# Kernel tuning notes

Hardware: AMD Instinct MI355X
Metric: run time of the kernel (lower is better)

## Reference

```python
import jax, jax.numpy as jnp
import numpy as np

B, H, NI, NQ = 4096, 1024, 4096, 2048


def setup_inputs() -> dict:
    key = jax.random.key(0)
    ks = jax.random.split(key, 12)
    state = jax.random.normal(ks[0], (B, H), jnp.float32)
    inputX = jax.random.normal(ks[1], (B, NI), jnp.float32)
    # one-hot next-question vector
    q_idx = jax.random.randint(ks[2], (B,), 0, NQ)
    inputY = jax.nn.one_hot(q_idx, NQ, dtype=jnp.float32)
    truth = jax.random.bernoulli(ks[3], 0.5, (B,)).astype(jnp.float32)
    # torch.nn.Linear default init: U(-1/sqrt(fan_in), 1/sqrt(fan_in)), weight (out,in)
    def lin(kw, kb, out_d, in_d):
        bound = 1.0 / np.sqrt(in_d)
        W = jax.random.uniform(kw, (out_d, in_d), jnp.float32, -bound, bound)
        b = jax.random.uniform(kb, (out_d,), jnp.float32, -bound, bound)
        return W, b
    W_t, b_t = lin(ks[4], ks[5], H, H)    # transfer: n_hidden -> n_hidden
    W_x, b_x = lin(ks[6], ks[7], H, NI)   # linear_x: n_input -> n_hidden
    W_y, b_y = lin(ks[8], ks[9], NQ, H)   # linear_y: n_hidden -> n_questions
    return {"state": state, "inputX": inputX, "inputY": inputY, "truth": truth,
            "W_t": W_t, "b_t": b_t, "W_x": W_x, "b_x": b_x, "W_y": W_y, "b_y": b_y}


def reference(state, inputX, inputY, truth, W_t, b_t, W_x, b_x, W_y, b_y):
    # two small linears + tanh -> new hidden state
    linM = state @ W_t.T + b_t                       # (B, H)
    linX = inputX @ W_x.T + b_x                      # (B, H)
    hidden = jnp.tanh(linM + linX)                   # (B, H)
    # prediction head: linear + sigmoid, mask-select via one-hot sum
    pred_output = jax.nn.sigmoid(hidden @ W_y.T + b_y)  # (B, NQ)
    pred = jnp.sum(pred_output * inputY, axis=1)        # (B,)
    # binary cross entropy, sum reduction; torch clamps log terms at -100
    log_p = jnp.maximum(jnp.log(pred), -100.0)
    log_1mp = jnp.maximum(jnp.log1p(-pred), -100.0)
    err = -jnp.sum(truth * log_p + (1.0 - truth) * log_1mp)
    return (pred, err, hidden)
```

## Files before the change

### kernel.cpp

```cpp
#include <hip/hip_runtime.h>
#include <stdint.h>
#include <math.h>

#define B_DIM 4096
#define H_DIM 1024
#define NI_DIM 4096
#define NQ_DIM 2048
#define K_DIM 5120
#define NKT 160

typedef __attribute__((ext_vector_type(8))) short short8;
typedef __attribute__((ext_vector_type(4))) float f32x4;

__device__ __forceinline__ unsigned short f2bf(float f) {
  unsigned u = __float_as_uint(f);
  u += 0x7FFFu + ((u >> 16) & 1u);
  return (unsigned short)(u >> 16);
}

__device__ __forceinline__ void gload_lds16(const void* g, void* l) {
  __builtin_amdgcn_global_load_lds(
      (__attribute__((address_space(1))) void*)(uintptr_t)g,
      (__attribute__((address_space(3))) void*)l, 16, 0, 0);
}

__global__ __launch_bounds__(256) void cast_tile(
    const float* __restrict__ src0, const float* __restrict__ src1,
    short* __restrict__ dst) {
  __shared__ __align__(16) short lds[4096];
  const unsigned bt = blockIdx.x;
  const int rowTile = bt / NKT;
  const int kt = bt % NKT;
  const float* src;
  long long srcBase;
  int cols;
  if (kt < 32) { src = src0; cols = 1024; srcBase = (long long)kt * 32; }
  else         { src = src1; cols = 4096; srcBase = (long long)(kt - 32) * 32; }
  const int tid = threadIdx.x;
#pragma unroll
  for (int half = 0; half < 2; ++half) {
    int c = tid + half * 256;
    int r = c >> 2, s = c & 3;
    long long sa = ((long long)(rowTile * 128 + r)) * cols + srcBase + s * 8;
    float4 v0 = *(const float4*)(src + sa);
    float4 v1 = *(const float4*)(src + sa + 4);
    short8 o;
    o[0] = (short)f2bf(v0.x); o[1] = (short)f2bf(v0.y);
    o[2] = (short)f2bf(v0.z); o[3] = (short)f2bf(v0.w);
    o[4] = (short)f2bf(v1.x); o[5] = (short)f2bf(v1.y);
    o[6] = (short)f2bf(v1.z); o[7] = (short)f2bf(v1.w);
    *(short8*)(&lds[(s * 128 + r) * 8]) = o;
  }
  __syncthreads();
  short* dtile = dst + (((long long)rowTile * NKT + kt) * 512) * 8;
#pragma unroll
  for (int half = 0; half < 2; ++half) {
    int c = tid + half * 256;
    *(short8*)(dtile + c * 8) = *(const short8*)(&lds[c * 8]);
  }
}

__global__ __launch_bounds__(256, 4) void gemm_splitk(
    const short* __restrict__ Xc, const short* __restrict__ Wc,
    float* __restrict__ P, int ntk) {
  __shared__ __align__(16) short As[2][4096];
  __shared__ __align__(16) short Bs[2][4096];
  const int tid = threadIdx.x;
  const int lane = tid & 63;
  const int wid = tid >> 6;
  const int wm = wid >> 1, wn = wid & 1;
  const int fr = lane & 15, fq = lane >> 4;

  const int nwg = gridDim.x;
  const int orig = blockIdx.x;
  const int cpx = nwg >> 3;
  const int swz = (orig & 7) * cpx + (orig >> 3);
  const int bz = swz >> 8;
  const int bm = (swz >> 3) & 31;
  const int bn = swz & 7;
  const int kt0 = bz * ntk;

  const int c0 = tid, c1 = tid + 256;
  const short* gA = Xc + (((long long)bm * NKT + kt0) << 12);
  const short* gB = Wc + (((long long)bn * NKT + kt0) << 12);

  f32x4 acc[4][4] = {};

  gload_lds16(gA + c0 * 8, &As[0][c0 * 8]);
  gload_lds16(gA + c1 * 8, &As[0][c1 * 8]);
  gload_lds16(gB + c0 * 8, &Bs[0][c0 * 8]);
  gload_lds16(gB + c1 * 8, &Bs[0][c1 * 8]);
  __syncthreads();

  int cur = 0;
  for (int t = 0; t < ntk; ++t) {
    if (t + 1 < ntk) {
      const short* nA = gA + (t + 1) * 4096;
      const short* nB = gB + (t + 1) * 4096;
      gload_lds16(nA + c0 * 8, &As[cur ^ 1][c0 * 8]);
      gload_lds16(nA + c1 * 8, &As[cur ^ 1][c1 * 8]);
      gload_lds16(nB + c0 * 8, &Bs[cur ^ 1][c0 * 8]);
      gload_lds16(nB + c1 * 8, &Bs[cur ^ 1][c1 * 8]);
    }
    const short* a_base = &As[cur][0];
    const short* b_base = &Bs[cur][0];
    short8 av[4], bv[4];
#pragma unroll
    for (int i = 0; i < 4; i++) {
      av[i] = *(const short8*)(a_base + (fq * 128 + wm * 64 + i * 16 + fr) * 8);
      bv[i] = *(const short8*)(b_base + (fq * 128 + wn * 64 + i * 16 + fr) * 8);
    }
#pragma unroll
    for (int mi = 0; mi < 4; mi++)
#pragma unroll
      for (int ni = 0; ni < 4; ni++)
        acc[mi][ni] = __builtin_amdgcn_mfma_f32_16x16x32_bf16(
            av[mi], bv[ni], acc[mi][ni], 0, 0, 0);
    __syncthreads();
    cur ^= 1;
  }

  float* Pp = P + (long long)bz * B_DIM * H_DIM;
  const int row0 = bm * 128 + wm * 64;
  const int col0 = bn * 128 + wn * 64;
#pragma unroll
  for (int ni = 0; ni < 4; ni++) {
    int col = col0 + ni * 16 + fr;
#pragma unroll
    for (int mi = 0; mi < 4; mi++) {
#pragma unroll
      for (int r = 0; r < 4; r++) {
        int row = row0 + mi * 16 + fq * 4 + r;
        Pp[(long long)row * H_DIM + col] = acc[mi][ni][r];
      }
    }
  }
}

__global__ __launch_bounds__(256) void reduce_bias_tanh(
    const float* __restrict__ P, const float* __restrict__ bt,
    const float* __restrict__ bx, float* __restrict__ hidden, int S) {
  const long long total4 = (long long)B_DIM * H_DIM / 4;
  for (long long e = (long long)blockIdx.x * 256 + threadIdx.x; e < total4;
       e += (long long)gridDim.x * 256) {
    long long base = e * 4;
    int col = (int)(base & (H_DIM - 1));
    float4 s = *(const float4*)(P + base);
    for (int z = 1; z < S; ++z) {
      float4 p = *(const float4*)(P + (long long)z * B_DIM * H_DIM + base);
      s.x += p.x; s.y += p.y; s.z += p.z; s.w += p.w;
    }
    float4 bt4 = *(const float4*)(bt + col);
    float4 bx4 = *(const float4*)(bx + col);
    hidden[base + 0] = tanhf(s.x + bt4.x + bx4.x);
    hidden[base + 1] = tanhf(s.y + bt4.y + bx4.y);
    hidden[base + 2] = tanhf(s.z + bt4.z + bx4.z);
    hidden[base + 3] = tanhf(s.w + bt4.w + bx4.w);
  }
}

__global__ __launch_bounds__(256) void pred_err(
    const float* __restrict__ hidden, const float* __restrict__ Y,
    const float* __restrict__ truth, const float* __restrict__ Wy,
    const float* __restrict__ by, float* __restrict__ predOut,
    float* __restrict__ bce) {
  const int b = blockIdx.x;
  const int tid = threadIdx.x;
  __shared__ int s_cnt;
  __shared__ int s_idx[8];
  __shared__ float s_val[8];
  __shared__ float s_red[4];
  if (tid == 0) s_cnt = 0;
  __syncthreads();
  const float4* Yr = (const float4*)(Y + (long long)b * NQ_DIM);
#pragma unroll
  for (int h = 0; h < NQ_DIM / 4 / 256; ++h) {
    int j = tid + h * 256;
    float4 v = Yr[j];
    if (v.x != 0.0f) { int p = atomicAdd(&s_cnt, 1); if (p < 8) { s_idx[p] = 4 * j;     s_val[p] = v.x; } }
    if (v.y != 0.0f) { int p = atomicAdd(&s_cnt, 1); if (p < 8) { s_idx[p] = 4 * j + 1; s_val[p] = v.y; } }
    if (v.z != 0.0f) { int p = atomicAdd(&s_cnt, 1); if (p < 8) { s_idx[p] = 4 * j + 2; s_val[p] = v.z; } }
    if (v.w != 0.0f) { int p = atomicAdd(&s_cnt, 1); if (p < 8) { s_idx[p] = 4 * j + 3; s_val[p] = v.w; } }
  }
  __syncthreads();
  int cnt = s_cnt < 8 ? s_cnt : 8;
  const float* Hr = hidden + (long long)b * H_DIM;
  float h0 = Hr[tid * 4 + 0], h1 = Hr[tid * 4 + 1];
  float h2 = Hr[tid * 4 + 2], h3 = Hr[tid * 4 + 3];
  float predv = 0.0f;
  for (int it = 0; it < cnt; ++it) {
    int q = s_idx[it];
    float4 w = *(const float4*)(Wy + (long long)q * H_DIM + tid * 4);
    float part = h0 * w.x + h1 * w.y + h2 * w.z + h3 * w.w;
#pragma unroll
    for (int off = 32; off > 0; off >>= 1) part += __shfl_down(part, off, 64);
    if ((tid & 63) == 0) s_red[tid >> 6] = part;
    __syncthreads();
    if (tid == 0) {
      float z = s_red[0] + s_red[1] + s_red[2] + s_red[3] + by[q];
      float p = 1.0f / (1.0f + expf(-z));
      predv += s_val[it] * p;
    }
    __syncthreads();
  }
  if (tid == 0) {
    predOut[b] = predv;
    float t = truth[b];
    float lp = fmaxf(logf(predv), -100.0f);
    float l1p = fmaxf(log1pf(-predv), -100.0f);
    bce[b] = -(t * lp + (1.0f - t) * l1p);
  }
}

__global__ __launch_bounds__(256) void reduce_err(
    const float* __restrict__ bce, float* __restrict__ errOut) {
  float s = 0.0f;
  for (int i = threadIdx.x; i < B_DIM; i += 256) s += bce[i];
#pragma unroll
  for (int off = 32; off > 0; off >>= 1) s += __shfl_down(s, off, 64);
  __shared__ float red[4];
  if ((threadIdx.x & 63) == 0) red[threadIdx.x >> 6] = s;
  __syncthreads();
  if (threadIdx.x == 0) errOut[0] = red[0] + red[1] + red[2] + red[3];
}

extern "C" void kernel_launch(void* const* d_in, const int* in_sizes, int n_in,
                              void* d_out, int out_size, void* d_ws, size_t ws_size,
                              hipStream_t stream) {
  (void)in_sizes; (void)n_in; (void)out_size;
  const float* state  = (const float*)d_in[0];
  const float* inputX = (const float*)d_in[1];
  const float* inputY = (const float*)d_in[2];
  const float* truth  = (const float*)d_in[3];
  const float* W_t    = (const float*)d_in[4];
  const float* b_t    = (const float*)d_in[5];
  const float* W_x    = (const float*)d_in[6];
  const float* b_x    = (const float*)d_in[7];
  const float* W_y    = (const float*)d_in[8];
  const float* b_y    = (const float*)d_in[9];

  const size_t XC_B = (size_t)B_DIM * K_DIM * 2;
  const size_t WC_B = (size_t)H_DIM * K_DIM * 2;
  const size_t PART = (size_t)B_DIM * H_DIM * 4;

  int S = 1;
  if (ws_size >= XC_B + WC_B + 4 * PART + 16384) S = 4;
  else if (ws_size >= XC_B + WC_B + 2 * PART + 16384) S = 2;

  short* Xc = (short*)d_ws;
  short* Wc = (short*)((char*)d_ws + XC_B);
  float* P  = (float*)((char*)d_ws + XC_B + WC_B);
  float* bce = (float*)((char*)d_ws + XC_B + WC_B + (size_t)S * PART);

  float* predOut = (float*)d_out;
  float* errOut  = predOut + B_DIM;
  float* hidden  = predOut + B_DIM + 1;

  cast_tile<<<(B_DIM / 128) * NKT, 256, 0, stream>>>(state, inputX, Xc);
  cast_tile<<<(H_DIM / 128) * NKT, 256, 0, stream>>>(W_t, W_x, Wc);

  gemm_splitk<<<256 * S, 256, 0, stream>>>(Xc, Wc, P, NKT / S);
  reduce_bias_tanh<<<2048, 256, 0, stream>>>(P, b_t, b_x, hidden, S);

  pred_err<<<B_DIM, 256, 0, stream>>>(hidden, inputY, truth, W_y, b_y, predOut, bce);
  reduce_err<<<1, 256, 0, stream>>>(bce, errOut);
}
```

Measured before the change: 109.0 us.

## Store split-K partials as bf16, fuse reduce/tanh into prediction kernel, merge casts

The split-K GEMM now writes its partial sums as bf16 through a swizzled LDS staging buffer, so global stores are coalesced and half the size. The separate reduce+tanh kernel is folded into the per-row prediction kernel, which sums the partials, applies bias and tanh, writes hidden, and reuses those values for the Wy dot product. The two cast launches are merged into one. This removes a launch and an fp32 round trip of partials and hidden, but rounding each partial to bf16 before summing loses accuracy.

New measurement: 92.99 us. 1.17x faster.

```diff
diff --git a/kernel.cpp b/kernel.cpp
--- a/kernel.cpp
+++ b/kernel.cpp
@@ -17,6 +17,9 @@
   u += 0x7FFFu + ((u >> 16) & 1u);
   return (unsigned short)(u >> 16);
 }
+__device__ __forceinline__ float bf2f(unsigned short s) {
+  return __uint_as_float(((unsigned)s) << 16);
+}
 
 __device__ __forceinline__ void gload_lds16(const void* g, void* l) {
   __builtin_amdgcn_global_load_lds(
@@ -24,18 +27,24 @@
       (__attribute__((address_space(3))) void*)l, 16, 0, 0);
 }
 
-__global__ __launch_bounds__(256) void cast_tile(
-    const float* __restrict__ src0, const float* __restrict__ src1,
-    short* __restrict__ dst) {
+__global__ __launch_bounds__(256) void cast_all(
+    const float* __restrict__ state, const float* __restrict__ inputX,
+    const float* __restrict__ Wt, const float* __restrict__ Wx,
+    short* __restrict__ Xc, short* __restrict__ Wc) {
   __shared__ __align__(16) short lds[4096];
-  const unsigned bt = blockIdx.x;
+  const int XTILES = (B_DIM / 128) * NKT;
+  int bt = blockIdx.x;
+  const float *s0, *s1;
+  short* dst;
+  if (bt < XTILES) { s0 = state; s1 = inputX; dst = Xc; }
+  else { bt -= XTILES; s0 = Wt; s1 = Wx; dst = Wc; }
   const int rowTile = bt / NKT;
   const int kt = bt % NKT;
   const float* src;
   long long srcBase;
   int cols;
-  if (kt < 32) { src = src0; cols = 1024; srcBase = (long long)kt * 32; }
-  else         { src = src1; cols = 4096; srcBase = (long long)(kt - 32) * 32; }
+  if (kt < 32) { src = s0; cols = 1024; srcBase = (long long)kt * 32; }
+  else         { src = s1; cols = 4096; srcBase = (long long)(kt - 32) * 32; }
   const int tid = threadIdx.x;
 #pragma unroll
   for (int half = 0; half < 2; ++half) {
@@ -60,11 +69,16 @@
   }
 }
 
+__device__ __forceinline__ int ep_swz(int col, int rw) {
+  int byte = col * 256 + rw * 2;
+  byte ^= ((col ^ (col >> 3)) & 7) << 4;
+  return byte;
+}
+
 __global__ __launch_bounds__(256, 4) void gemm_splitk(
     const short* __restrict__ Xc, const short* __restrict__ Wc,
-    float* __restrict__ P, int ntk) {
-  __shared__ __align__(16) short As[2][4096];
-  __shared__ __align__(16) short Bs[2][4096];
+    short* __restrict__ P, int ntk) {
+  __shared__ __align__(16) short SH[16384];
   const int tid = threadIdx.x;
   const int lane = tid & 63;
   const int wid = tid >> 6;
@@ -86,24 +100,26 @@
 
   f32x4 acc[4][4] = {};
 
-  gload_lds16(gA + c0 * 8, &As[0][c0 * 8]);
-  gload_lds16(gA + c1 * 8, &As[0][c1 * 8]);
-  gload_lds16(gB + c0 * 8, &Bs[0][c0 * 8]);
-  gload_lds16(gB + c1 * 8, &Bs[0][c1 * 8]);
+  gload_lds16(gA + c0 * 8, &SH[c0 * 8]);
+  gload_lds16(gA + c1 * 8, &SH[c1 * 8]);
+  gload_lds16(gB + c0 * 8, &SH[8192 + c0 * 8]);
+  gload_lds16(gB + c1 * 8, &SH[8192 + c1 * 8]);
   __syncthreads();
 
   int cur = 0;
   for (int t = 0; t < ntk; ++t) {
     if (t + 1 < ntk) {
-      const short* nA = gA + (t + 1) * 4096;
-      const short* nB = gB + (t + 1) * 4096;
-      gload_lds16(nA + c0 * 8, &As[cur ^ 1][c0 * 8]);
-      gload_lds16(nA + c1 * 8, &As[cur ^ 1][c1 * 8]);
-      gload_lds16(nB + c0 * 8, &Bs[cur ^ 1][c0 * 8]);
-      gload_lds16(nB + c1 * 8, &Bs[cur ^ 1][c1 * 8]);
-    }
-    const short* a_base = &As[cur][0];
-    const short* b_base = &Bs[cur][0];
+      const short* nA = gA + (long long)(t + 1) * 4096;
+      const short* nB = gB + (long long)(t + 1) * 4096;
+      short* lA = &SH[(cur ^ 1) * 4096];
+      short* lB = &SH[8192 + (cur ^ 1) * 4096];
+      gload_lds16(nA + c0 * 8, lA + c0 * 8);
+      gload_lds16(nA + c1 * 8, lA + c1 * 8);
+      gload_lds16(nB + c0 * 8, lB + c0 * 8);
+      gload_lds16(nB + c1 * 8, lB + c1 * 8);
+    }
+    const short* a_base = &SH[cur * 4096];
+    const short* b_base = &SH[8192 + cur * 4096];
     short8 av[4], bv[4];
 #pragma unroll
     for (int i = 0; i < 4; i++) {
@@ -120,50 +136,42 @@
     cur ^= 1;
   }
 
-  float* Pp = P + (long long)bz * B_DIM * H_DIM;
-  const int row0 = bm * 128 + wm * 64;
-  const int col0 = bn * 128 + wn * 64;
 #pragma unroll
   for (int ni = 0; ni < 4; ni++) {
-    int col = col0 + ni * 16 + fr;
+    int col = wn * 64 + ni * 16 + fr;
 #pragma unroll
     for (int mi = 0; mi < 4; mi++) {
-#pragma unroll
-      for (int r = 0; r < 4; r++) {
-        int row = row0 + mi * 16 + fq * 4 + r;
-        Pp[(long long)row * H_DIM + col] = acc[mi][ni][r];
-      }
-    }
-  }
-}
-
-__global__ __launch_bounds__(256) void reduce_bias_tanh(
-    const float* __restrict__ P, const float* __restrict__ bt,
-    const float* __restrict__ bx, float* __restrict__ hidden, int S) {
-  const long long total4 = (long long)B_DIM * H_DIM / 4;
-  for (long long e = (long long)blockIdx.x * 256 + threadIdx.x; e < total4;
-       e += (long long)gridDim.x * 256) {
-    long long base = e * 4;
-    int col = (int)(base & (H_DIM - 1));
-    float4 s = *(const float4*)(P + base);
-    for (int z = 1; z < S; ++z) {
-      float4 p = *(const float4*)(P + (long long)z * B_DIM * H_DIM + base);
-      s.x += p.x; s.y += p.y; s.z += p.z; s.w += p.w;
-    }
-    float4 bt4 = *(const float4*)(bt + col);
-    float4 bx4 = *(const float4*)(bx + col);
-    hidden[base + 0] = tanhf(s.x + bt4.x + bx4.x);
-    hidden[base + 1] = tanhf(s.y + bt4.y + bx4.y);
-    hidden[base + 2] = tanhf(s.z + bt4.z + bx4.z);
-    hidden[base + 3] = tanhf(s.w + bt4.w + bx4.w);
-  }
-}
-
-__global__ __launch_bounds__(256) void pred_err(
-    const float* __restrict__ hidden, const float* __restrict__ Y,
+      int rw = wm * 64 + mi * 16 + fq * 4;
+      unsigned lo = (unsigned)f2bf(acc[mi][ni][0]) |
+                    ((unsigned)f2bf(acc[mi][ni][1]) << 16);
+      unsigned hi = (unsigned)f2bf(acc[mi][ni][2]) |
+                    ((unsigned)f2bf(acc[mi][ni][3]) << 16);
+      uint2 pk; pk.x = lo; pk.y = hi;
+      *(uint2*)((char*)SH + ep_swz(col, rw)) = pk;
+    }
+  }
+  __syncthreads();
+  short* Pp = P + (long long)bz * B_DIM * H_DIM;
+#pragma unroll
+  for (int h = 0; h < 8; ++h) {
+    int chunk = tid + h * 256;
+    int r = chunk >> 4;
+    int j = chunk & 15;
+    short8 o;
+#pragma unroll
+    for (int k = 0; k < 8; ++k) {
+      o[k] = *(const short*)((char*)SH + ep_swz(j * 8 + k, r));
+    }
+    *(short8*)(Pp + (long long)(bm * 128 + r) * H_DIM + bn * 128 + j * 8) = o;
+  }
+}
+
+__global__ __launch_bounds__(256) void fuse_row(
+    const short* __restrict__ P, const float* __restrict__ bt,
+    const float* __restrict__ bx, const float* __restrict__ Y,
     const float* __restrict__ truth, const float* __restrict__ Wy,
     const float* __restrict__ by, float* __restrict__ predOut,
-    float* __restrict__ bce) {
+    float* __restrict__ hidden, float* __restrict__ bce, int S) {
   const int b = blockIdx.x;
   const int tid = threadIdx.x;
   __shared__ int s_cnt;
@@ -171,11 +179,31 @@
   __shared__ float s_val[8];
   __shared__ float s_red[4];
   if (tid == 0) s_cnt = 0;
+
+  const int c = tid * 4;
+  float s0 = 0.f, s1 = 0.f, s2 = 0.f, s3 = 0.f;
+  for (int z = 0; z < S; ++z) {
+    const short* Pr = P + ((long long)z * B_DIM + b) * H_DIM + c;
+    uint2 u = *(const uint2*)Pr;
+    s0 += bf2f((unsigned short)(u.x & 0xffff));
+    s1 += bf2f((unsigned short)(u.x >> 16));
+    s2 += bf2f((unsigned short)(u.y & 0xffff));
+    s3 += bf2f((unsigned short)(u.y >> 16));
+  }
+  float4 bt4 = *(const float4*)(bt + c);
+  float4 bx4 = *(const float4*)(bx + c);
+  float h0 = tanhf(s0 + bt4.x + bx4.x);
+  float h1 = tanhf(s1 + bt4.y + bx4.y);
+  float h2 = tanhf(s2 + bt4.z + bx4.z);
+  float h3 = tanhf(s3 + bt4.w + bx4.w);
+  float* Hr = hidden + (long long)b * H_DIM + c;
+  Hr[0] = h0; Hr[1] = h1; Hr[2] = h2; Hr[3] = h3;
+
   __syncthreads();
   const float4* Yr = (const float4*)(Y + (long long)b * NQ_DIM);
 #pragma unroll
-  for (int h = 0; h < NQ_DIM / 4 / 256; ++h) {
-    int j = tid + h * 256;
+  for (int hh = 0; hh < NQ_DIM / 4 / 256; ++hh) {
+    int j = tid + hh * 256;
     float4 v = Yr[j];
     if (v.x != 0.0f) { int p = atomicAdd(&s_cnt, 1); if (p < 8) { s_idx[p] = 4 * j;     s_val[p] = v.x; } }
     if (v.y != 0.0f) { int p = atomicAdd(&s_cnt, 1); if (p < 8) { s_idx[p] = 4 * j + 1; s_val[p] = v.y; } }
@@ -184,13 +212,10 @@
   }
   __syncthreads();
   int cnt = s_cnt < 8 ? s_cnt : 8;
-  const float* Hr = hidden + (long long)b * H_DIM;
-  float h0 = Hr[tid * 4 + 0], h1 = Hr[tid * 4 + 1];
-  float h2 = Hr[tid * 4 + 2], h3 = Hr[tid * 4 + 3];
   float predv = 0.0f;
   for (int it = 0; it < cnt; ++it) {
     int q = s_idx[it];
-    float4 w = *(const float4*)(Wy + (long long)q * H_DIM + tid * 4);
+    float4 w = *(const float4*)(Wy + (long long)q * H_DIM + c);
     float part = h0 * w.x + h1 * w.y + h2 * w.z + h3 * w.w;
 #pragma unroll
     for (int off = 32; off > 0; off >>= 1) part += __shfl_down(part, off, 64);
@@ -241,7 +266,7 @@
 
   const size_t XC_B = (size_t)B_DIM * K_DIM * 2;
   const size_t WC_B = (size_t)H_DIM * K_DIM * 2;
-  const size_t PART = (size_t)B_DIM * H_DIM * 4;
+  const size_t PART = (size_t)B_DIM * H_DIM * 2;
 
   int S = 1;
   if (ws_size >= XC_B + WC_B + 4 * PART + 16384) S = 4;
@@ -249,19 +274,19 @@
 
   short* Xc = (short*)d_ws;
   short* Wc = (short*)((char*)d_ws + XC_B);
-  float* P  = (float*)((char*)d_ws + XC_B + WC_B);
+  short* P  = (short*)((char*)d_ws + XC_B + WC_B);
   float* bce = (float*)((char*)d_ws + XC_B + WC_B + (size_t)S * PART);
 
   float* predOut = (float*)d_out;
   float* errOut  = predOut + B_DIM;
   float* hidden  = predOut + B_DIM + 1;
 
-  cast_tile<<<(B_DIM / 128) * NKT, 256, 0, stream>>>(state, inputX, Xc);
-  cast_tile<<<(H_DIM / 128) * NKT, 256, 0, stream>>>(W_t, W_x, Wc);
+  cast_all<<<(B_DIM / 128 + H_DIM / 128) * NKT, 256, 0, stream>>>(
+      state, inputX, W_t, W_x, Xc, Wc);
 
   gemm_splitk<<<256 * S, 256, 0, stream>>>(Xc, Wc, P, NKT / S);
-  reduce_bias_tanh<<<2048, 256, 0, stream>>>(P, b_t, b_x, hidden, S);
-
-  pred_err<<<B_DIM, 256, 0, stream>>>(hidden, inputY, truth, W_y, b_y, predOut, bce);
+
+  fuse_row<<<B_DIM, 256, 0, stream>>>(P, b_t, b_x, inputY, truth, W_y, b_y,
+                                      predOut, hidden, bce, S);
   reduce_err<<<1, 256, 0, stream>>>(bce, errOut);
 }
```
